# Kernel optimization log

Hardware: AMD Instinct MI355X
Metric: run time of the kernel (lower is better)

## Reference

```python
import jax, jax.numpy as jnp
import numpy as np

B, S, D = 1, 2048, 1024
HK, DK = 8, 64
HV, DV = 16, 64
KEY_DIM = HK * DK          # 512
VAL_DIM = HV * DV          # 1024
CONV_DIM = 2 * KEY_DIM + VAL_DIM  # 2048
KW = 4                     # conv kernel width
E, TOPK, I_MOE = 8, 2, 512
EPS = 1e-6


def rms_norm(x, w, eps=EPS):
    xf = x.astype(jnp.float32)
    y = xf * jax.lax.rsqrt(jnp.mean(xf * xf, axis=-1, keepdims=True) + eps)
    return (y * (1.0 + w.astype(jnp.float32))).astype(x.dtype)


def l2norm(x, eps=1e-6):
    return x * jax.lax.rsqrt(jnp.sum(x * x, axis=-1, keepdims=True) + eps)


def setup_inputs() -> dict:
    key = jax.random.key(0)
    ks = jax.random.split(key, 16)
    n = lambda k, shp, s=0.02: (jax.random.normal(k, shp, dtype=jnp.float32) * s)
    return {
        'x': jax.random.normal(ks[0], (B, S, D), dtype=jnp.float32),
        'state': jnp.zeros((B, HV, DK, DV), dtype=jnp.float32),
        'conv_state': jnp.zeros((B, KW - 1, CONV_DIM), dtype=jnp.float32),
        'in_proj_qkv': n(ks[1], (D, CONV_DIM)),
        'in_proj_z': n(ks[2], (D, VAL_DIM)),
        'in_proj_a': n(ks[3], (D, HV)),
        'in_proj_b': n(ks[4], (D, HV)),
        'conv1d_weight': n(ks[5], (CONV_DIM, KW)),
        'dt_bias': jnp.ones((HV,), dtype=jnp.float32),
        'A_log': jnp.zeros((HV,), dtype=jnp.float32),
        'norm_weight': jnp.zeros((VAL_DIM,), dtype=jnp.float32),
        'out_proj': n(ks[6], (VAL_DIM, D)),
        'router_weight': n(ks[7], (E, D)),
        'expert_gate_up': n(ks[8], (E, 2 * I_MOE, D)),
        'expert_down': n(ks[9], (E, D, I_MOE)),
        'shared_gate': n(ks[10], (D, VAL_DIM)),
        'shared_up': n(ks[11], (D, VAL_DIM)),
        'shared_down': n(ks[12], (VAL_DIM, D)),
        'shared_expert_gate': n(ks[13], (D, 1)),
        'attention_norm_weight': jnp.zeros((D,), dtype=jnp.float32),
        'ffn_norm_weight': jnp.zeros((D,), dtype=jnp.float32),
        'linear_layer_idx': 0,
    }


def reference(x, state, conv_state, in_proj_qkv, in_proj_z, in_proj_a, in_proj_b,
              conv1d_weight, dt_bias, A_log, norm_weight, out_proj,
              router_weight, expert_gate_up, expert_down, shared_gate, shared_up,
              shared_down, shared_expert_gate, attention_norm_weight,
              ffn_norm_weight, linear_layer_idx):
    bsz, seqlen, dim = x.shape
    h = rms_norm(x, attention_norm_weight)

    # ---- Gated DeltaNet linear attention (prefill) ----
    qkv = h @ in_proj_qkv                    # [B,S,CONV_DIM]
    z = h @ in_proj_z                        # [B,S,VAL_DIM]
    a = h @ in_proj_a                        # [B,S,HV]
    b = h @ in_proj_b                        # [B,S,HV]

    # causal depthwise conv1d with rolling cache, then SiLU
    seq = jnp.concatenate([conv_state, qkv], axis=1)     # [B,S+KW-1,C]
    new_conv_state = seq[:, -(KW - 1):, :]
    xc = jnp.swapaxes(seq, 1, 2)                         # [B,C,S+KW-1]
    wk = conv1d_weight[:, None, :]                       # [C,1,KW]
    conv = jax.lax.conv_general_dilated(
        xc, wk, window_strides=(1,), padding='VALID',
        dimension_numbers=('NCH', 'OIH', 'NCH'), feature_group_count=CONV_DIM)
    qkv = jax.nn.silu(jnp.swapaxes(conv, 1, 2))          # [B,S,C]

    q, k, v = jnp.split(qkv, [KEY_DIM, 2 * KEY_DIM], axis=-1)
    q = l2norm(q.reshape(bsz, seqlen, HK, DK))
    k = l2norm(k.reshape(bsz, seqlen, HK, DK))
    rep = HV // HK
    q = jnp.repeat(q, rep, axis=2) * (DK ** -0.5)        # [B,S,HV,DK]
    k = jnp.repeat(k, rep, axis=2)
    v = v.reshape(bsz, seqlen, HV, DV)

    beta = jax.nn.sigmoid(b)                             # [B,S,HV]
    g = -jnp.exp(A_log) * jax.nn.softplus(a + dt_bias)   # log decay
    decay = jnp.exp(g)                                   # [B,S,HV]

    def step(St, inp):
        qt, kt, vt, dt_, bt = inp                        # per-token slices
        St = St * dt_[..., None, None]                   # gated decay
        mem = jnp.einsum('bhk,bhkv->bhv', kt, St)        # retrieve
        delta = (vt - mem) * bt[..., None]               # delta rule
        St = St + jnp.einsum('bhk,bhv->bhkv', kt, delta)
        ot = jnp.einsum('bhk,bhkv->bhv', qt, St)
        return St, ot

    xs = (jnp.moveaxis(q, 1, 0), jnp.moveaxis(k, 1, 0), jnp.moveaxis(v, 1, 0),
          jnp.moveaxis(decay, 1, 0), jnp.moveaxis(beta, 1, 0))
    new_state, o = jax.lax.scan(step, state, xs)
    o = jnp.moveaxis(o, 0, 1)                            # [B,S,HV,DV]

    # gated RMSNorm per value head, gate = silu(z)
    nw = (1.0 + norm_weight.astype(jnp.float32)).reshape(HV, DV)
    of = o.astype(jnp.float32)
    of = of * jax.lax.rsqrt(jnp.mean(of * of, axis=-1, keepdims=True) + EPS) * nw
    o = (of * jax.nn.silu(z.reshape(bsz, seqlen, HV, DV).astype(jnp.float32))).astype(x.dtype)
    attn_out = o.reshape(bsz, seqlen, VAL_DIM) @ out_proj
    x = x + attn_out

    # ---- MoE FFN with shared expert ----
    hf = rms_norm(x, ffn_norm_weight)
    t = hf.reshape(-1, dim)                              # [T,D]
    T = t.shape[0]
    logits = t @ router_weight.T                         # [T,E]
    probs = jax.nn.softmax(logits.astype(jnp.float32), axis=-1)
    vals, idx = jax.lax.top_k(probs, TOPK)
    vals = vals / jnp.sum(vals, axis=-1, keepdims=True)  # renormalized top-k
    wdense = jnp.zeros((T, E), jnp.float32).at[jnp.arange(T)[:, None], idx].set(vals)

    gu = jnp.einsum('td,eid->tei', t, expert_gate_up)    # [T,E,2I]
    gate, up = jnp.split(gu, 2, axis=-1)
    act = jax.nn.silu(gate) * up                         # [T,E,I]
    eo = jnp.einsum('tei,edi->ted', act, expert_down)    # [T,E,D]
    routed = jnp.einsum('ted,te->td', eo, wdense.astype(eo.dtype))

    sh = (jax.nn.silu(t @ shared_gate) * (t @ shared_up)) @ shared_down
    sh = sh * jax.nn.sigmoid(t @ shared_expert_gate)

    moe_out = (routed + sh).reshape(bsz, seqlen, dim)
    x = x + moe_out
    return x, new_state, new_conv_state
```

## Files before the change

### kernel.cpp

```cpp
#include <hip/hip_runtime.h>
#include <stdint.h>

typedef _Float16 f16;
typedef __attribute__((ext_vector_type(8))) _Float16 f16x8;
typedef __attribute__((ext_vector_type(4))) float f32x4;

#define DEV static __device__ __forceinline__

DEV float siluf(float x){ return x/(1.f+expf(-x)); }

DEV void load_lds16(const f16* g, f16* l){
  __builtin_amdgcn_global_load_lds(
      (const __attribute__((address_space(1))) void*)g,
      (__attribute__((address_space(3))) void*)l, 16, 0, 0);
}

__global__ __launch_bounds__(256)
void prep_kernel(const float* __restrict__ qkvw, const float* __restrict__ zw,
                 const float* __restrict__ opw, const float* __restrict__ sgw,
                 const float* __restrict__ suw, const float* __restrict__ sdw,
                 const float* __restrict__ guw, const float* __restrict__ dww,
                 f16* __restrict__ wqkvz, f16* __restrict__ wop, f16* __restrict__ wsgu,
                 f16* __restrict__ wsd, f16* __restrict__ wgu, f16* __restrict__ wdn)
{
  int b = blockIdx.x, tid = threadIdx.x;
  if (b >= 7168){
    if (b < 9216){
      size_t base = ((size_t)(b-7168))*4096 + (size_t)tid*16;
      long e = base>>20; long i = (base>>10)&1023; long d = base&1023;
      long ri = (i<512) ? ((i>>6)*128 + (i&63)) : (((i&511)>>6)*128 + 64 + (i&63));
      size_t dbase = ((size_t)e<<20) + ((size_t)ri<<10) + d;
      #pragma unroll
      for (int u=0;u<16;u++) wgu[dbase+u] = (f16)guw[base+u];
    } else {
      size_t base = ((size_t)(b-9216))*4096 + (size_t)tid*16;
      #pragma unroll
      for (int u=0;u<16;u++) wdn[base+u] = (f16)dww[base+u];
    }
    return;
  }
  const float* src; f16* dst; int N; int rowOff; int tile; int mode=0;
  if (b < 2048){ src=qkvw; dst=wqkvz; N=2048; rowOff=0;    tile=b; }
  else if (b < 3072){ src=zw;  dst=wqkvz; N=1024; rowOff=2048; tile=b-2048; }
  else if (b < 4096){ src=opw; dst=wop;  N=1024; rowOff=0;    tile=b-3072; }
  else if (b < 5120){ src=sgw; dst=wsgu; N=1024; rowOff=0;    tile=b-4096; mode=1; }
  else if (b < 6144){ src=suw; dst=wsgu; N=1024; rowOff=0;    tile=b-5120; mode=2; }
  else              { src=sdw; dst=wsd;  N=1024; rowOff=0;    tile=b-6144; }
  __shared__ float t32[32][33];
  int ntiles = N/32;
  int k0 = (tile/ntiles)*32, n0 = (tile%ntiles)*32;
  int rr = tid>>5, cc = tid&31;
  #pragma unroll
  for (int u=0;u<4;u++) t32[rr+u*8][cc] = src[(size_t)(k0+rr+u*8)*N + n0+cc];
  __syncthreads();
  #pragma unroll
  for (int u=0;u<4;u++){
    int vr = n0 + rr + u*8;
    int drow = rowOff + vr;
    if (mode==1) drow = (vr>>6)*128 + (vr&63);
    else if (mode==2) drow = (vr>>6)*128 + 64 + (vr&63);
    dst[(size_t)drow*1024 + k0+cc] = (f16)t32[cc][rr+u*8];
  }
}

__global__ __launch_bounds__(256)
void rms1(const float* __restrict__ xin, const float* __restrict__ w, f16* __restrict__ hb)
{
  __shared__ float red[4];
  int t = blockIdx.x, tid = threadIdx.x;
  const float* row = xin + (long)t*1024;
  float vals[4]; float ss=0.f;
  #pragma unroll
  for (int u=0;u<4;u++){ vals[u]=row[tid+256*u]; ss += vals[u]*vals[u]; }
  #pragma unroll
  for (int m=1;m<64;m<<=1) ss += __shfl_xor(ss,m);
  if ((tid&63)==0) red[tid>>6]=ss;
  __syncthreads();
  float sc = rsqrtf((red[0]+red[1]+red[2]+red[3])*(1.f/1024.f) + 1e-6f);
  #pragma unroll
  for (int u=0;u<4;u++){
    int d = tid+256*u;
    hb[(long)t*1024+d] = (f16)(vals[u]*sc*(1.f+w[d]));
  }
}

__global__ __launch_bounds__(256)
void rms2(const float* __restrict__ xin, const float* __restrict__ w,
          const float* __restrict__ rw, const float* __restrict__ seg,
          f16* __restrict__ hb,
          int* __restrict__ cnt, int* __restrict__ etok, int* __restrict__ eslot,
          float* __restrict__ ew, float* __restrict__ sig)
{
  __shared__ float red[4];
  __shared__ float rbuf[9][4];
  int t = blockIdx.x, tid = threadIdx.x, lane = tid&63, wv = tid>>6;
  const float* row = xin + (long)t*1024;
  float vals[4]; float ss=0.f;
  #pragma unroll
  for (int u=0;u<4;u++){ vals[u]=row[tid+256*u]; ss += vals[u]*vals[u]; }
  #pragma unroll
  for (int m=1;m<64;m<<=1) ss += __shfl_xor(ss,m);
  if (lane==0) red[wv]=ss;
  __syncthreads();
  float sc = rsqrtf((red[0]+red[1]+red[2]+red[3])*(1.f/1024.f) + 1e-6f);
  float p[9];
  #pragma unroll
  for (int e=0;e<9;e++) p[e]=0.f;
  #pragma unroll
  for (int u=0;u<4;u++){
    int d = tid+256*u;
    float v = vals[u]*sc*(1.f+w[d]);
    hb[(long)t*1024+d] = (f16)v;
    #pragma unroll
    for (int e=0;e<8;e++) p[e] += v*rw[e*1024+d];
    p[8] += v*seg[d];
  }
  #pragma unroll
  for (int e=0;e<9;e++)
    #pragma unroll
    for (int m=1;m<64;m<<=1) p[e] += __shfl_xor(p[e], m);
  if (lane==0){
    #pragma unroll
    for (int e=0;e<9;e++) rbuf[e][wv]=p[e];
  }
  __syncthreads();
  if (tid==0){
    float pl[9];
    #pragma unroll
    for (int e=0;e<9;e++) pl[e]=rbuf[e][0]+rbuf[e][1]+rbuf[e][2]+rbuf[e][3];
    float mx = pl[0];
    for (int e=1;e<8;e++) mx = fmaxf(mx,pl[e]);
    float pe[8];
    for (int e=0;e<8;e++) pe[e]=expf(pl[e]-mx);
    int i0=0; for (int e=1;e<8;e++) if (pe[e]>pe[i0]) i0=e;
    int i1 = (i0==0)?1:0;
    for (int e=0;e<8;e++) if (e!=i0 && pe[e]>pe[i1]) i1=e;
    float denom = pe[i0]+pe[i1];
    float w0 = pe[i0]/denom, w1 = pe[i1]/denom;
    int p0 = atomicAdd(&cnt[i0],1);
    etok[i0*2048+p0]=t; eslot[i0*2048+p0]=0; ew[i0*2048+p0]=w0;
    int p1 = atomicAdd(&cnt[i1],1);
    etok[i1*2048+p1]=t; eslot[i1*2048+p1]=1; ew[i1*2048+p1]=w1;
    sig[t] = 1.f/(1.f+expf(-pl[8]));
  }
}

constexpr int GM_PLAIN=0, GM_ADDX=1, GM_GUF=2, GM_DOWN=3, GM_SHD=4, GM_SGUF=5;

template<int MODE>
__global__ __launch_bounds__(256)
void gemm_k(const f16* __restrict__ A, long strideA,
            const f16* __restrict__ B, long strideB,
            int K, int lda, int ldb,
            float* __restrict__ Cf, f16* __restrict__ Cb, int ldc, long strideCb,
            const float* __restrict__ xadd,
            const int* __restrict__ tok, const int* __restrict__ cntp,
            const int* __restrict__ slot, const float* __restrict__ wgt,
            const float* __restrict__ sig)
{
  constexpr bool FUSED = (MODE==GM_GUF || MODE==GM_SGUF);
  __shared__ f16 As[128*64];
  __shared__ f16 Bs[128*64];
  __shared__ int ltok[128];
  const int e = blockIdx.z;
  const int m0 = blockIdx.y*128, n0 = blockIdx.x*128;
  int cnt = 0x7fffffff;
  if (MODE==GM_GUF || MODE==GM_DOWN){
    cnt = cntp[e];
    if (m0 >= cnt) return;
  }
  const f16* Ap = A + (long)e*strideA;
  const f16* Bp = B + (long)e*strideB;
  const int tid = threadIdx.x, lane = tid&63, wv = tid>>6;
  if (MODE==GM_GUF){
    if (tid < 128){
      int p = m0 + tid;
      ltok[tid] = (p < cnt) ? tok[e*2048 + p] : 0;
    }
    __syncthreads();
  }
  const int srow = wv*8 + (lane>>3);
  const int scol = (lane&7)*8;
  long arow[4];
  #pragma unroll
  for (int i=0;i<4;i++){
    int r = srow + i*32;
    arow[i] = (MODE==GM_GUF) ? (long)ltok[r] : (long)(m0 + r);
  }
  f32x4 acc[4][4];
  #pragma unroll
  for (int mi=0;mi<4;mi++)
    #pragma unroll
    for (int ni=0;ni<4;ni++)
      acc[mi][ni] = (f32x4){0.f,0.f,0.f,0.f};

  for (int k0=0;k0<K;k0+=64){
    __syncthreads();
    #pragma unroll
    for (int i=0;i<4;i++){
      int r = srow + i*32;
      load_lds16(Ap + arow[i]*lda + k0 + scol, &As[r*64 + scol]);
      load_lds16(Bp + (long)(n0 + r)*ldb + k0 + scol, &Bs[r*64 + scol]);
    }
    __syncthreads();
    #pragma unroll
    for (int kk=0;kk<64;kk+=32){
      f16x8 af[4], bf[4];
      #pragma unroll
      for (int mi=0;mi<4;mi++){
        int row = (wv&1)*64 + mi*16 + (lane&15);
        af[mi] = *(const f16x8*)&As[row*64 + kk + (lane>>4)*8];
      }
      #pragma unroll
      for (int ni=0;ni<4;ni++){
        int row = FUSED ? (ni*32 + (wv>>1)*16 + (lane&15))
                        : ((wv>>1)*64 + ni*16 + (lane&15));
        bf[ni] = *(const f16x8*)&Bs[row*64 + kk + (lane>>4)*8];
      }
      #pragma unroll
      for (int mi=0;mi<4;mi++)
        #pragma unroll
        for (int ni=0;ni<4;ni++)
          acc[mi][ni] = __builtin_amdgcn_mfma_f32_16x16x32_f16(af[mi], bf[ni], acc[mi][ni], 0,0,0);
    }
  }
  if (FUSED){
    #pragma unroll
    for (int mi=0;mi<4;mi++){
      #pragma unroll
      for (int r=0;r<4;r++){
        int rowl = (wv&1)*64 + mi*16 + (lane>>4)*4 + r;
        int pos = m0 + rowl;
        #pragma unroll
        for (int pi=0;pi<2;pi++){
          int v = (n0>>1) + pi*32 + (wv>>1)*16 + (lane&15);
          float g = acc[mi][pi][r], u = acc[mi][pi+2][r];
          f16 a = (f16)(siluf(g)*u);
          if (MODE==GM_GUF) Cb[(long)e*strideCb + (long)pos*ldc + v] = a;
          else              Cb[(long)pos*ldc + v] = a;
        }
      }
    }
  } else {
    #pragma unroll
    for (int mi=0;mi<4;mi++){
      #pragma unroll
      for (int r=0;r<4;r++){
        int rowl = (wv&1)*64 + mi*16 + (lane>>4)*4 + r;
        int pos = m0 + rowl;
        int tk=0, sl=0; float wrow=0.f;
        if (MODE==GM_DOWN){
          if (pos < cnt){ tk = tok[e*2048+pos]; sl = slot[e*2048+pos]; wrow = wgt[e*2048+pos]; }
        }
        #pragma unroll
        for (int ni=0;ni<4;ni++){
          int col = n0 + (wv>>1)*64 + ni*16 + (lane&15);
          float v = acc[mi][ni][r];
          if (MODE==GM_PLAIN){
            Cf[(long)pos*ldc + col] = v;
          } else if (MODE==GM_ADDX){
            long idx = (long)pos*ldc + col;
            Cf[idx] = v + xadd[idx];
          } else if (MODE==GM_DOWN){
            if (pos < cnt) Cf[(long)sl*2097152 + (long)tk*1024 + col] = v*wrow;
          } else {
            Cf[(long)pos*ldc + col] = v*sig[pos];
          }
        }
      }
    }
  }
}

__global__ __launch_bounds__(256)
void ab_kernel(const f16* __restrict__ hb, const float* __restrict__ Wa,
               const float* __restrict__ Wbp, const float* __restrict__ dtb,
               const float* __restrict__ alog,
               float* __restrict__ gg, float* __restrict__ bbet)
{
  __shared__ float hrow[1024];
  __shared__ float part[256];
  int t = blockIdx.x, tid = threadIdx.x;
  #pragma unroll
  for (int u=0;u<4;u++){ int d = tid+256*u; hrow[d] = (float)hb[(long)t*1024+d]; }
  __syncthreads();
  int o = tid & 31;
  int r = tid >> 5;
  const float* W = (o<16) ? Wa : Wbp;
  int col = o & 15;
  float s = 0.f;
  for (int d=r; d<1024; d+=8) s += hrow[d]*W[d*16+col];
  part[tid] = s;
  __syncthreads();
  if (tid < 32){
    float tot=0.f;
    #pragma unroll
    for (int q=0;q<8;q++) tot += part[q*32 + tid];
    if (tid<16){
      float a = tot + dtb[tid];
      float sp = (a>20.f)? a : log1pf(expf(a));
      gg[t*16+tid] = -expf(alog[tid])*sp;
    } else {
      bbet[t*16+(tid-16)] = 1.f/(1.f+expf(-tot));
    }
  }
}

__global__ __launch_bounds__(256)
void conv_kernel(const float* __restrict__ qkvz, const float* __restrict__ cs,
                 const float* __restrict__ cw,
                 float* __restrict__ qn, float* __restrict__ kn,
                 float* __restrict__ vb, float* __restrict__ conv_out)
{
  int t = blockIdx.y;
  int c = blockIdx.x*256 + threadIdx.x;
  f32x4 w4 = *(const f32x4*)&cw[c*4];
  float acc = 0.f;
  #pragma unroll
  for (int j=0;j<4;j++){
    int s = t + j;
    float xv = (s<3) ? cs[s*2048 + c] : qkvz[(long)(s-3)*3072 + c];
    acc += w4[j]*xv;
  }
  float sv = siluf(acc);
  if (c < 1024){
    float ssq = sv*sv;
    #pragma unroll
    for (int m=1;m<64;m<<=1) ssq += __shfl_xor(ssq, m);
    float y = sv*rsqrtf(ssq + 1e-6f);
    if (c < 512) qn[(long)t*512 + c] = y*0.125f;
    else         kn[(long)t*512 + (c-512)] = y;
  } else {
    vb[(long)t*1024 + (c-1024)] = sv;
  }
  if (t >= 2045) conv_out[(t-2045)*2048 + c] = qkvz[(long)t*3072 + c];
}

__global__ __launch_bounds__(256)
void scan_pre(const float* __restrict__ kn, const float* __restrict__ vg,
              const float* __restrict__ gg, const float* __restrict__ bb,
              float* __restrict__ U0, f16* __restrict__ WbB,
              float* __restrict__ MT, float* __restrict__ NT)
{
  __shared__ f16 Kh[64][72];
  __shared__ f16 KrT[64][72];
  __shared__ f16 Amh[64][72];
  __shared__ float XT[64][68];
  __shared__ f16 Xh[64][72];
  __shared__ float cexp[64], gam[64], rlast[64], betl[64];
  const int task = blockIdx.x;
  const int h = task>>5, c = task&31, hk = h>>1;
  const int tid = threadIdx.x, lane = tid&63, wv = tid>>6;
  const long tb = (long)task*4096;

  if (wv==0){
    float g = gg[(c*64+lane)*16 + h];
    #pragma unroll
    for (int off=1; off<64; off<<=1){
      float tpp = __shfl_up(g, off);
      if (lane >= off) g += tpp;
    }
    cexp[lane] = g;
    betl[lane] = bb[(c*64+lane)*16 + h];
  }
  __syncthreads();
  if (tid<64){ gam[tid]=expf(cexp[tid]); rlast[tid]=expf(cexp[63]-cexp[tid]); }
  __syncthreads();
  for (int u=0;u<16;u++){
    int e2=u*256+tid; int t=e2>>6, x=e2&63;
    float kx = kn[(long)(c*64+t)*512 + hk*64 + x];
    Kh[t][x] = (f16)kx;
    KrT[x][t] = (f16)(rlast[t]*kx);
  }
  __syncthreads();
  {
    int mt = wv;
    for (int nt=0;nt<4;nt++){
      f32x4 acc = {0.f,0.f,0.f,0.f};
      #pragma unroll
      for (int kk=0;kk<64;kk+=32){
        f16x8 a = *(const f16x8*)&Kh[mt*16 + (lane&15)][kk + (lane>>4)*8];
        f16x8 bB = *(const f16x8*)&Kh[nt*16 + (lane&15)][kk + (lane>>4)*8];
        acc = __builtin_amdgcn_mfma_f32_16x16x32_f16(a, bB, acc, 0,0,0);
      }
      #pragma unroll
      for (int r=0;r<4;r++){
        int t = mt*16 + (lane>>4)*4 + r;
        int i = nt*16 + (lane&15);
        float v = (i<t) ? betl[t]*expf(cexp[t]-cexp[i])*acc[r] : 0.f;
        Amh[t][i] = (f16)v;
      }
    }
  }

  for (int pass=0; pass<2; pass++){
    for (int u=0;u<18;u++) ((f16*)Xh)[u*256+tid] = (f16)0.f;
    for (int u=0;u<16;u++){
      int e2=u*256+tid; int t=e2>>6, col=e2&63;
      float v = (pass==0) ? betl[t]*vg[(long)(c*64+t)*1024 + h*64 + col]
                          : betl[t]*gam[t]*kn[(long)(c*64+t)*512 + hk*64 + col];
      XT[col][t] = v;
    }
    __syncthreads();

    for (int b4=0;b4<4;b4++){
      if (tid<64){
        int col = tid;
        float xr[16];
        #pragma unroll
        for (int j=0;j<16;j+=4){
          f32x4 v = *(const f32x4*)&XT[col][b4*16+j];
          xr[j]=v.x; xr[j+1]=v.y; xr[j+2]=v.z; xr[j+3]=v.w;
        }
        #pragma unroll
        for (int t=1;t<16;t++){
          float a = xr[t];
          #pragma unroll
          for (int i=0;i<t;i++) a -= (float)Amh[b4*16+t][b4*16+i]*xr[i];
          xr[t] = a;
        }
        #pragma unroll
        for (int j=0;j<16;j+=4)
          *(f32x4*)&XT[col][b4*16+j] = (f32x4){xr[j],xr[j+1],xr[j+2],xr[j+3]};
        f16x8 h0, h1;
        #pragma unroll
        for (int j=0;j<8;j++){ h0[j]=(f16)xr[j]; h1[j]=(f16)xr[8+j]; }
        *(f16x8*)&Xh[col][b4*16]   = h0;
        *(f16x8*)&Xh[col][b4*16+8] = h1;
        if (pass==0){
          #pragma unroll
          for (int j=0;j<16;j++) U0[tb + (b4*16+j)*64 + col] = xr[j];
        } else {
          #pragma unroll
          for (int j=0;j<16;j++) WbB[tb + (b4*16+j)*64 + col] = (f16)xr[j];
        }
      }
      __syncthreads();
      if (b4<3){
        int ntiles = 4*(3-b4);
        for (int idx=wv; idx<ntiles; idx+=4){
          int mtile = idx & 3;
          int ntile = idx >> 2;
          int tp0 = 16*(b4+1) + ntile*16;
          f16x8 a  = *(const f16x8*)&Xh[mtile*16 + (lane&15)][b4*16 + (lane>>4)*8];
          f16x8 bB = *(const f16x8*)&Amh[tp0 + (lane&15)][b4*16 + (lane>>4)*8];
          f32x4 acc = {0.f,0.f,0.f,0.f};
          acc = __builtin_amdgcn_mfma_f32_16x16x32_f16(a, bB, acc, 0,0,0);
          #pragma unroll
          for (int r=0;r<4;r++){
            int colr = mtile*16 + (lane>>4)*4 + r;
            int tp = tp0 + (lane&15);
            XT[colr][tp] -= acc[r];
          }
        }
      }
      __syncthreads();
    }
    for (int idx=wv; idx<16; idx+=4){
      int mtile = idx & 3, ntile = idx >> 2;
      f32x4 acc = {0.f,0.f,0.f,0.f};
      #pragma unroll
      for (int kk=0;kk<64;kk+=32){
        f16x8 a  = *(const f16x8*)&Xh[mtile*16 + (lane&15)][kk + (lane>>4)*8];
        f16x8 bB = *(const f16x8*)&KrT[ntile*16 + (lane&15)][kk + (lane>>4)*8];
        acc = __builtin_amdgcn_mfma_f32_16x16x32_f16(a, bB, acc, 0,0,0);
      }
      #pragma unroll
      for (int r=0;r<4;r++){
        int m = mtile*16 + (lane>>4)*4 + r;
        int n = ntile*16 + (lane&15);
        if (pass==0) NT[tb + m*64 + n] = acc[r];
        else         MT[tb + m*64 + n] = ((n==m)?gam[63]:0.f) - acc[r];
      }
    }
    __syncthreads();
  }
}

__global__ __launch_bounds__(256)
void scan_seq(const float* __restrict__ st_in, const float* __restrict__ MT,
              const float* __restrict__ NT, float* __restrict__ SS,
              float* __restrict__ st_out)
{
  __shared__ float Mb[2][64*64];
  __shared__ float Nb[2][16*64];
  __shared__ float Sl[64][16];
  const int h = blockIdx.x>>2, vgq = blockIdx.x&3;
  const int tid = threadIdx.x, lane = tid&63, wv = tid>>6;
  const long hb0 = (long)h*32*4096;
  {
    int kx = tid>>2, j0 = (tid&3)*4;
    f32x4 s = *(const f32x4*)&st_in[h*4096 + kx*64 + vgq*16 + j0];
    *(f32x4*)&Sl[kx][j0] = s;
  }
  f32x4 mreg[4]; f32x4 nreg;
  #pragma unroll
  for (int u=0;u<4;u++) mreg[u] = *(const f32x4*)&MT[hb0 + (u*256+tid)*4];
  nreg = *(const f32x4*)&NT[hb0 + vgq*1024 + tid*4];
  #pragma unroll
  for (int u=0;u<4;u++) *(f32x4*)&Mb[0][(u*256+tid)*4] = mreg[u];
  *(f32x4*)&Nb[0][tid*4] = nreg;
  __syncthreads();

  const int kx = tid>>2, j0 = (tid&3)*4;
  for (int c=0;c<32;c++){
    const int buf = c&1;
    const long tb = hb0 + (long)c*4096;
    *(f32x4*)&SS[tb + kx*64 + vgq*16 + j0] = *(const f32x4*)&Sl[kx][j0];
    if (c<31){
      const long tb1 = tb + 4096;
      #pragma unroll
      for (int u=0;u<4;u++) mreg[u] = *(const f32x4*)&MT[tb1 + (u*256+tid)*4];
      nreg = *(const f32x4*)&NT[tb1 + vgq*1024 + tid*4];
    }
    f32x4 acc = {0.f,0.f,0.f,0.f};
    #pragma unroll 16
    for (int b=0;b<64;b++){
      float m = Mb[buf][b*64 + lane];
      f32x4 s4 = *(const f32x4*)&Sl[b][wv*4];
      acc.x += m*s4.x; acc.y += m*s4.y; acc.z += m*s4.z; acc.w += m*s4.w;
    }
    __syncthreads();
    Sl[lane][wv*4+0] = acc.x + Nb[buf][(wv*4+0)*64 + lane];
    Sl[lane][wv*4+1] = acc.y + Nb[buf][(wv*4+1)*64 + lane];
    Sl[lane][wv*4+2] = acc.z + Nb[buf][(wv*4+2)*64 + lane];
    Sl[lane][wv*4+3] = acc.w + Nb[buf][(wv*4+3)*64 + lane];
    if (c<31){
      #pragma unroll
      for (int u=0;u<4;u++) *(f32x4*)&Mb[buf^1][(u*256+tid)*4] = mreg[u];
      *(f32x4*)&Nb[buf^1][tid*4] = nreg;
    }
    __syncthreads();
  }
  *(f32x4*)&st_out[h*4096 + kx*64 + vgq*16 + j0] = *(const f32x4*)&Sl[kx][j0];
}

__global__ __launch_bounds__(256)
void scan_out(const float* __restrict__ qn, const float* __restrict__ kn,
              const float* __restrict__ gg, const float* __restrict__ U0,
              const f16* __restrict__ WbB, const float* __restrict__ SS,
              const float* __restrict__ qkvz, const float* __restrict__ nw,
              f16* __restrict__ obuf)
{
  __shared__ f16 Kh[64][72];
  __shared__ f16 Qh[64][72];
  __shared__ f16 Wbh[64][72];
  __shared__ f16 Bmh[64][72];
  __shared__ f16 STh[64][72];
  __shared__ f16 UTh[64][72];
  __shared__ float cexp[64], gam[64];
  const int task = blockIdx.x;
  const int h = task>>5, c = task&31, hk = h>>1;
  const int tid = threadIdx.x, lane = tid&63, wv = tid>>6;
  const long tb = (long)task*4096;

  if (wv==0){
    float g = gg[(c*64+lane)*16 + h];
    #pragma unroll
    for (int off=1; off<64; off<<=1){
      float tpp = __shfl_up(g, off);
      if (lane >= off) g += tpp;
    }
    cexp[lane]=g; gam[lane]=expf(g);
  }
  __syncthreads();
  for (int u=0;u<16;u++){
    int e2=u*256+tid; int t=e2>>6, x=e2&63;
    float kx = kn[(long)(c*64+t)*512 + hk*64 + x];
    float qx = qn[(long)(c*64+t)*512 + hk*64 + x];
    Kh[t][x]=(f16)kx;
    Qh[t][x]=(f16)qx;
    Wbh[t][x] = WbB[tb + t*64 + x];
    STh[x][t] = (f16)SS[tb + t*64 + x];
  }
  __syncthreads();
  {
    int mt = wv;
    for (int nt=0;nt<4;nt++){
      f32x4 acc={0.f,0.f,0.f,0.f};
      #pragma unroll
      for (int kk=0;kk<64;kk+=32){
        f16x8 a  = *(const f16x8*)&Qh[mt*16+(lane&15)][kk+(lane>>4)*8];
        f16x8 bB = *(const f16x8*)&Kh[nt*16+(lane&15)][kk+(lane>>4)*8];
        acc = __builtin_amdgcn_mfma_f32_16x16x32_f16(a,bB,acc,0,0,0);
      }
      #pragma unroll
      for (int r=0;r<4;r++){
        int t = mt*16+(lane>>4)*4+r;
        int i = nt*16+(lane&15);
        float v = (i<=t)? expf(cexp[t]-cexp[i])*acc[r] : 0.f;
        Bmh[t][i] = (f16)v;
      }
    }
  }
  __syncthreads();
  {
    int mt = wv;
    for (int nt=0;nt<4;nt++){
      f32x4 acc={0.f,0.f,0.f,0.f};
      #pragma unroll
      for (int kk=0;kk<64;kk+=32){
        f16x8 a  = *(const f16x8*)&Wbh[mt*16+(lane&15)][kk+(lane>>4)*8];
        f16x8 bB = *(const f16x8*)&STh[nt*16+(lane&15)][kk+(lane>>4)*8];
        acc = __builtin_amdgcn_mfma_f32_16x16x32_f16(a,bB,acc,0,0,0);
      }
      #pragma unroll
      for (int r=0;r<4;r++){
        int t = mt*16+(lane>>4)*4+r;
        int v = nt*16+(lane&15);
        float uv = U0[tb + t*64 + v] - acc[r];
        UTh[v][t] = (f16)uv;
      }
    }
    for (int u=0;u<16;u++){
      int e2=u*256+tid; int t=e2>>6, x=e2&63;
      Qh[t][x] = (f16)(gam[t]*(float)Qh[t][x]);
    }
  }
  __syncthreads();
  {
    int mt = wv;
    f32x4 acc[4];
    for (int nt=0;nt<4;nt++){
      acc[nt]=(f32x4){0.f,0.f,0.f,0.f};
      #pragma unroll
      for (int kk=0;kk<64;kk+=32){
        f16x8 a  = *(const f16x8*)&Qh[mt*16+(lane&15)][kk+(lane>>4)*8];
        f16x8 bB = *(const f16x8*)&STh[nt*16+(lane&15)][kk+(lane>>4)*8];
        acc[nt] = __builtin_amdgcn_mfma_f32_16x16x32_f16(a,bB,acc[nt],0,0,0);
      }
      #pragma unroll
      for (int kk=0;kk<64;kk+=32){
        f16x8 a  = *(const f16x8*)&Bmh[mt*16+(lane&15)][kk+(lane>>4)*8];
        f16x8 bB = *(const f16x8*)&UTh[nt*16+(lane&15)][kk+(lane>>4)*8];
        acc[nt] = __builtin_amdgcn_mfma_f32_16x16x32_f16(a,bB,acc[nt],0,0,0);
      }
    }
    #pragma unroll
    for (int r=0;r<4;r++){
      float ss = acc[0][r]*acc[0][r] + acc[1][r]*acc[1][r]
               + acc[2][r]*acc[2][r] + acc[3][r]*acc[3][r];
      ss += __shfl_xor(ss,1); ss += __shfl_xor(ss,2);
      ss += __shfl_xor(ss,4); ss += __shfl_xor(ss,8);
      float scale = rsqrtf(ss*(1.f/64.f) + 1e-6f);
      int t = mt*16 + (lane>>4)*4 + r;
      int tg = c*64 + t;
      #pragma unroll
      for (int nt=0;nt<4;nt++){
        int v = nt*16 + (lane&15);
        float z = qkvz[(long)tg*3072 + 2048 + h*64 + v];
        float val = acc[nt][r]*scale*(1.f+nw[h*64+v])*siluf(z);
        obuf[(long)tg*1024 + h*64 + v] = (f16)val;
      }
    }
  }
}

__global__ __launch_bounds__(256)
void fin_kernel(const float* __restrict__ x2, const float* __restrict__ eo2,
                const float* __restrict__ sh, float* __restrict__ outx)
{
  long idx = (long)blockIdx.x*256 + threadIdx.x;
  outx[idx] = x2[idx] + eo2[idx] + eo2[idx + 2097152] + sh[idx];
}

extern "C" void kernel_launch(void* const* d_in, const int* in_sizes, int n_in,
                              void* d_out, int out_size, void* d_ws, size_t ws_size,
                              hipStream_t stream)
{
  (void)in_sizes; (void)n_in; (void)out_size; (void)ws_size;
  const float* x      = (const float*)d_in[0];
  const float* state  = (const float*)d_in[1];
  const float* cstate = (const float*)d_in[2];
  const float* w_qkv  = (const float*)d_in[3];
  const float* w_z    = (const float*)d_in[4];
  const float* w_a    = (const float*)d_in[5];
  const float* w_b    = (const float*)d_in[6];
  const float* convw  = (const float*)d_in[7];
  const float* dtb    = (const float*)d_in[8];
  const float* alog   = (const float*)d_in[9];
  const float* normw  = (const float*)d_in[10];
  const float* w_op   = (const float*)d_in[11];
  const float* rw     = (const float*)d_in[12];
  const float* w_gu   = (const float*)d_in[13];
  const float* w_dn   = (const float*)d_in[14];
  const float* w_sg   = (const float*)d_in[15];
  const float* w_su   = (const float*)d_in[16];
  const float* w_sd   = (const float*)d_in[17];
  const float* w_seg  = (const float*)d_in[18];
  const float* anw    = (const float*)d_in[19];
  const float* fnw    = (const float*)d_in[20];

  char* ws = (char*)d_ws;
  size_t off = 0;
  auto alloc = [&](size_t bytes)->char*{
    char* p = ws + off; off += (bytes + 255) & ~(size_t)255; return p;
  };
  f16*  wTqkvz = (f16*)alloc((size_t)3072*1024*2);
  f16*  wTop   = (f16*)alloc((size_t)1024*1024*2);
  f16*  wTsgu  = (f16*)alloc((size_t)2048*1024*2);
  f16*  wTsd   = (f16*)alloc((size_t)1024*1024*2);
  f16*  wGUc   = (f16*)alloc((size_t)8*1024*1024*2);
  f16*  wDNc   = (f16*)alloc((size_t)8*1024*512*2);
  f16*  hbuf   = (f16*)alloc((size_t)2048*1024*2);
  float* qkvz  = (float*)alloc((size_t)2048*3072*4);
  float* qn    = (float*)alloc((size_t)2048*512*4);
  float* kn    = (float*)alloc((size_t)2048*512*4);
  float* vb    = (float*)alloc((size_t)2048*1024*4);
  float* gg    = (float*)alloc((size_t)2048*16*4);
  float* bbuf  = (float*)alloc((size_t)2048*16*4);
  float* U0    = (float*)alloc((size_t)512*4096*4);
  f16*  WbB    = (f16*)alloc((size_t)512*4096*2);
  float* MT    = (float*)alloc((size_t)512*4096*4);
  float* NT    = (float*)alloc((size_t)512*4096*4);
  float* SS    = (float*)alloc((size_t)512*4096*4);
  float* x2    = (float*)alloc((size_t)2048*1024*4);
  f16*  hfb    = (f16*)alloc((size_t)2048*1024*2);
  int*  cnt    = (int*)alloc(256);
  int*  etok   = (int*)alloc((size_t)8*2048*4);
  int*  eslot  = (int*)alloc((size_t)8*2048*4);
  float* ew    = (float*)alloc((size_t)8*2048*4);
  float* sigb  = (float*)alloc((size_t)2048*4);
  f16*  obuf  = hbuf;
  f16*  sactb = (f16*)qn;
  float* shb  = vb;
  f16*  actb  = (f16*)U0;
  float* eo2  = (float*)((char*)U0 + (size_t)16777216);

  float* out_x = (float*)d_out;
  float* out_state = out_x + 2097152;
  float* out_conv = out_state + 65536;

  hipMemsetAsync((void*)cnt, 0, 64, stream);
  prep_kernel<<<10240, 256, 0, stream>>>(w_qkv, w_z, w_op, w_sg, w_su, w_sd, w_gu, w_dn,
                                         wTqkvz, wTop, wTsgu, wTsd, wGUc, wDNc);
  rms1<<<2048, 256, 0, stream>>>(x, anw, hbuf);
  gemm_k<GM_PLAIN><<<dim3(24,16,1), 256, 0, stream>>>(hbuf, 0, wTqkvz, 0, 1024, 1024, 1024,
        qkvz, nullptr, 3072, 0, nullptr, nullptr, nullptr, nullptr, nullptr, nullptr);
  ab_kernel<<<2048, 256, 0, stream>>>(hbuf, w_a, w_b, dtb, alog, gg, bbuf);
  conv_kernel<<<dim3(8,2048), 256, 0, stream>>>(qkvz, cstate, convw, qn, kn, vb, out_conv);
  scan_pre<<<512, 256, 0, stream>>>(kn, vb, gg, bbuf, U0, WbB, MT, NT);
  scan_seq<<<64, 256, 0, stream>>>(state, MT, NT, SS, out_state);
  scan_out<<<512, 256, 0, stream>>>(qn, kn, gg, U0, WbB, SS, qkvz, normw, obuf);
  gemm_k<GM_ADDX><<<dim3(8,16,1), 256, 0, stream>>>(obuf, 0, wTop, 0, 1024, 1024, 1024,
        x2, nullptr, 1024, 0, x, nullptr, nullptr, nullptr, nullptr, nullptr);
  rms2<<<2048, 256, 0, stream>>>(x2, fnw, rw, w_seg, hfb, cnt, etok, eslot, ew, sigb);
  gemm_k<GM_GUF><<<dim3(8,16,8), 256, 0, stream>>>(hfb, 0, wGUc, (long)1024*1024, 1024, 1024, 1024,
        nullptr, actb, 512, (long)2048*512, nullptr, etok, cnt, nullptr, nullptr, nullptr);
  gemm_k<GM_DOWN><<<dim3(8,16,8), 256, 0, stream>>>(actb, (long)2048*512, wDNc, (long)1024*512,
        512, 512, 512,
        eo2, nullptr, 1024, 0, nullptr, etok, cnt, eslot, ew, nullptr);
  gemm_k<GM_SGUF><<<dim3(16,16,1), 256, 0, stream>>>(hfb, 0, wTsgu, 0, 1024, 1024, 1024,
        nullptr, sactb, 1024, 0, nullptr, nullptr, nullptr, nullptr, nullptr, nullptr);
  gemm_k<GM_SHD><<<dim3(8,16,1), 256, 0, stream>>>(sactb, 0, wTsd, 0, 1024, 1024, 1024,
        shb, nullptr, 1024, 0, nullptr, nullptr, nullptr, nullptr, nullptr, sigb);
  fin_kernel<<<8192, 256, 0, stream>>>(x2, eo2, shb, out_x);
}
```

Baseline: 516.0 us.

## Store qkvz projection in fp16 and build expert routing lists in one block

Result: faster. 481.0 us (-6.8%).

```diff
diff --git a/kernel.cpp b/kernel.cpp
--- a/kernel.cpp
+++ b/kernel.cpp
@@ -87,9 +87,7 @@
 __global__ __launch_bounds__(256)
 void rms2(const float* __restrict__ xin, const float* __restrict__ w,
           const float* __restrict__ rw, const float* __restrict__ seg,
-          f16* __restrict__ hb,
-          int* __restrict__ cnt, int* __restrict__ etok, int* __restrict__ eslot,
-          float* __restrict__ ew, float* __restrict__ sig)
+          f16* __restrict__ hb, float4* __restrict__ tkbuf, float* __restrict__ sig)
 {
   __shared__ float red[4];
   __shared__ float rbuf[9][4];
@@ -136,16 +134,40 @@
     int i1 = (i0==0)?1:0;
     for (int e=0;e<8;e++) if (e!=i0 && pe[e]>pe[i1]) i1=e;
     float denom = pe[i0]+pe[i1];
-    float w0 = pe[i0]/denom, w1 = pe[i1]/denom;
-    int p0 = atomicAdd(&cnt[i0],1);
-    etok[i0*2048+p0]=t; eslot[i0*2048+p0]=0; ew[i0*2048+p0]=w0;
-    int p1 = atomicAdd(&cnt[i1],1);
-    etok[i1*2048+p1]=t; eslot[i1*2048+p1]=1; ew[i1*2048+p1]=w1;
+    float4 outp;
+    outp.x = __int_as_float(i0);
+    outp.y = __int_as_float(i1);
+    outp.z = pe[i0]/denom;
+    outp.w = pe[i1]/denom;
+    tkbuf[t] = outp;
     sig[t] = 1.f/(1.f+expf(-pl[8]));
   }
 }
 
-constexpr int GM_PLAIN=0, GM_ADDX=1, GM_GUF=2, GM_DOWN=3, GM_SHD=4, GM_SGUF=5;
+__global__ __launch_bounds__(1024)
+void route_build(const float4* __restrict__ tkbuf,
+                 int* __restrict__ cnt, int* __restrict__ etok,
+                 int* __restrict__ eslot, float* __restrict__ ew)
+{
+  __shared__ int lcnt[8];
+  int tid = threadIdx.x;
+  if (tid<8) lcnt[tid]=0;
+  __syncthreads();
+  #pragma unroll
+  for (int u=0;u<2;u++){
+    int t = tid + u*1024;
+    float4 pk = tkbuf[t];
+    int i0 = __float_as_int(pk.x), i1 = __float_as_int(pk.y);
+    int p0 = atomicAdd(&lcnt[i0],1);
+    etok[i0*2048+p0]=t; eslot[i0*2048+p0]=0; ew[i0*2048+p0]=pk.z;
+    int p1 = atomicAdd(&lcnt[i1],1);
+    etok[i1*2048+p1]=t; eslot[i1*2048+p1]=1; ew[i1*2048+p1]=pk.w;
+  }
+  __syncthreads();
+  if (tid<8) cnt[tid]=lcnt[tid];
+}
+
+constexpr int GM_PLAIN16=0, GM_ADDX=1, GM_GUF=2, GM_DOWN=3, GM_SHD=4, GM_SGUF=5;
 
 template<int MODE>
 __global__ __launch_bounds__(256)
@@ -256,8 +278,8 @@
         for (int ni=0;ni<4;ni++){
           int col = n0 + (wv>>1)*64 + ni*16 + (lane&15);
           float v = acc[mi][ni][r];
-          if (MODE==GM_PLAIN){
-            Cf[(long)pos*ldc + col] = v;
+          if (MODE==GM_PLAIN16){
+            Cb[(long)pos*ldc + col] = (f16)v;
           } else if (MODE==GM_ADDX){
             long idx = (long)pos*ldc + col;
             Cf[idx] = v + xadd[idx];
@@ -307,7 +329,7 @@
 }
 
 __global__ __launch_bounds__(256)
-void conv_kernel(const float* __restrict__ qkvz, const float* __restrict__ cs,
+void conv_kernel(const f16* __restrict__ qkvz, const float* __restrict__ cs,
                  const float* __restrict__ cw,
                  float* __restrict__ qn, float* __restrict__ kn,
                  float* __restrict__ vb, float* __restrict__ conv_out)
@@ -319,7 +341,7 @@
   #pragma unroll
   for (int j=0;j<4;j++){
     int s = t + j;
-    float xv = (s<3) ? cs[s*2048 + c] : qkvz[(long)(s-3)*3072 + c];
+    float xv = (s<3) ? cs[s*2048 + c] : (float)qkvz[(long)(s-3)*3072 + c];
     acc += w4[j]*xv;
   }
   float sv = siluf(acc);
@@ -333,7 +355,7 @@
   } else {
     vb[(long)t*1024 + (c-1024)] = sv;
   }
-  if (t >= 2045) conv_out[(t-2045)*2048 + c] = qkvz[(long)t*3072 + c];
+  if (t >= 2045) conv_out[(t-2045)*2048 + c] = (float)qkvz[(long)t*3072 + c];
 }
 
 __global__ __launch_bounds__(256)
@@ -539,7 +561,7 @@
 void scan_out(const float* __restrict__ qn, const float* __restrict__ kn,
               const float* __restrict__ gg, const float* __restrict__ U0,
               const f16* __restrict__ WbB, const float* __restrict__ SS,
-              const float* __restrict__ qkvz, const float* __restrict__ nw,
+              const f16* __restrict__ qkvz, const float* __restrict__ nw,
               f16* __restrict__ obuf)
 {
   __shared__ f16 Kh[64][72];
@@ -648,7 +670,7 @@
       #pragma unroll
       for (int nt=0;nt<4;nt++){
         int v = nt*16 + (lane&15);
-        float z = qkvz[(long)tg*3072 + 2048 + h*64 + v];
+        float z = (float)qkvz[(long)tg*3072 + 2048 + h*64 + v];
         float val = acc[nt][r]*scale*(1.f+nw[h*64+v])*siluf(z);
         obuf[(long)tg*1024 + h*64 + v] = (f16)val;
       }
@@ -703,7 +725,7 @@
   f16*  wGUc   = (f16*)alloc((size_t)8*1024*1024*2);
   f16*  wDNc   = (f16*)alloc((size_t)8*1024*512*2);
   f16*  hbuf   = (f16*)alloc((size_t)2048*1024*2);
-  float* qkvz  = (float*)alloc((size_t)2048*3072*4);
+  f16*  qkvzh  = (f16*)alloc((size_t)2048*3072*2);
   float* qn    = (float*)alloc((size_t)2048*512*4);
   float* kn    = (float*)alloc((size_t)2048*512*4);
   float* vb    = (float*)alloc((size_t)2048*1024*4);
@@ -721,6 +743,7 @@
   int*  eslot  = (int*)alloc((size_t)8*2048*4);
   float* ew    = (float*)alloc((size_t)8*2048*4);
   float* sigb  = (float*)alloc((size_t)2048*4);
+  float4* tkbuf= (float4*)alloc((size_t)2048*16);
   f16*  obuf  = hbuf;
   f16*  sactb = (f16*)qn;
   float* shb  = vb;
@@ -731,20 +754,20 @@
   float* out_state = out_x + 2097152;
   float* out_conv = out_state + 65536;
 
-  hipMemsetAsync((void*)cnt, 0, 64, stream);
   prep_kernel<<<10240, 256, 0, stream>>>(w_qkv, w_z, w_op, w_sg, w_su, w_sd, w_gu, w_dn,
                                          wTqkvz, wTop, wTsgu, wTsd, wGUc, wDNc);
   rms1<<<2048, 256, 0, stream>>>(x, anw, hbuf);
-  gemm_k<GM_PLAIN><<<dim3(24,16,1), 256, 0, stream>>>(hbuf, 0, wTqkvz, 0, 1024, 1024, 1024,
-        qkvz, nullptr, 3072, 0, nullptr, nullptr, nullptr, nullptr, nullptr, nullptr);
+  gemm_k<GM_PLAIN16><<<dim3(24,16,1), 256, 0, stream>>>(hbuf, 0, wTqkvz, 0, 1024, 1024, 1024,
+        nullptr, qkvzh, 3072, 0, nullptr, nullptr, nullptr, nullptr, nullptr, nullptr);
   ab_kernel<<<2048, 256, 0, stream>>>(hbuf, w_a, w_b, dtb, alog, gg, bbuf);
-  conv_kernel<<<dim3(8,2048), 256, 0, stream>>>(qkvz, cstate, convw, qn, kn, vb, out_conv);
+  conv_kernel<<<dim3(8,2048), 256, 0, stream>>>(qkvzh, cstate, convw, qn, kn, vb, out_conv);
   scan_pre<<<512, 256, 0, stream>>>(kn, vb, gg, bbuf, U0, WbB, MT, NT);
   scan_seq<<<64, 256, 0, stream>>>(state, MT, NT, SS, out_state);
-  scan_out<<<512, 256, 0, stream>>>(qn, kn, gg, U0, WbB, SS, qkvz, normw, obuf);
+  scan_out<<<512, 256, 0, stream>>>(qn, kn, gg, U0, WbB, SS, qkvzh, normw, obuf);
   gemm_k<GM_ADDX><<<dim3(8,16,1), 256, 0, stream>>>(obuf, 0, wTop, 0, 1024, 1024, 1024,
         x2, nullptr, 1024, 0, x, nullptr, nullptr, nullptr, nullptr, nullptr);
-  rms2<<<2048, 256, 0, stream>>>(x2, fnw, rw, w_seg, hfb, cnt, etok, eslot, ew, sigb);
+  rms2<<<2048, 256, 0, stream>>>(x2, fnw, rw, w_seg, hfb, tkbuf, sigb);
+  route_build<<<1, 1024, 0, stream>>>(tkbuf, cnt, etok, eslot, ew);
   gemm_k<GM_GUF><<<dim3(8,16,8), 256, 0, stream>>>(hfb, 0, wGUc, (long)1024*1024, 1024, 1024, 1024,
         nullptr, actb, 512, (long)2048*512, nullptr, etok, cnt, nullptr, nullptr, nullptr);
   gemm_k<GM_DOWN><<<dim3(8,16,8), 256, 0, stream>>>(actb, (long)2048*512, wDNc, (long)1024*512,
```
